# Kernel optimization log

Measured on AMD Instinct MI355X. Metric: run time of the kernel, lower is better.

Reference implementation:

```python
import jax, jax.numpy as jnp
import numpy as np

D_MODEL = 1024
NUM_HEADS = 16
D_K = D_MODEL // NUM_HEADS
NEG_INF = -1.0e9


def setup_inputs() -> dict:
    key = jax.random.key(0)
    ks = jax.random.split(key, 12)
    B, S = 2, 2048
    s = 1.0 / np.sqrt(D_MODEL)
    return {
        "q": jax.random.normal(ks[0], (B, S, D_MODEL), jnp.float32),
        "k": jax.random.normal(ks[1], (B, S, D_MODEL), jnp.float32),
        "v": jax.random.normal(ks[2], (B, S, D_MODEL), jnp.float32),
        "encoder_mask": jnp.ones((B, 1, 1, S), jnp.int32),
        "W_q": jax.random.normal(ks[3], (D_MODEL, D_MODEL), jnp.float32) * s,
        "b_q": jnp.zeros((D_MODEL,), jnp.float32),
        "W_k": jax.random.normal(ks[4], (D_MODEL, D_MODEL), jnp.float32) * s,
        "b_k": jnp.zeros((D_MODEL,), jnp.float32),
        "W_v": jax.random.normal(ks[5], (D_MODEL, D_MODEL), jnp.float32) * s,
        "b_v": jnp.zeros((D_MODEL,), jnp.float32),
        "W_o": jax.random.normal(ks[6], (D_MODEL, D_MODEL), jnp.float32) * s,
        "b_o": jnp.zeros((D_MODEL,), jnp.float32),
    }


def reference(q, k, v, encoder_mask, W_q, b_q, W_k, b_k, W_v, b_v, W_o, b_o):
    B, S, _ = q.shape
    # projections (torch Linear: x @ W^T + b)
    def proj(x, W, b):
        y = x @ W.T + b
        return y.reshape(B, -1, NUM_HEADS, D_K).transpose(0, 2, 1, 3)  # [B,H,S,dk]

    Q = proj(q, W_q, b_q)
    K = proj(k, W_k, b_k)
    V = proj(v, W_v, b_v)

    scores = jnp.einsum("bhqd,bhkd->bhqk", Q, K) / jnp.sqrt(jnp.float32(D_K))
    scores = jnp.where(encoder_mask == 0, NEG_INF, scores)
    # NOTE: source module computes softmax(scores) but then (bug) multiplies
    # the raw masked scores by V; softmax result is dead code, so we skip it.
    attn_out = jnp.einsum("bhqk,bhkd->bhqd", scores, V)
    attn_out = attn_out.transpose(0, 2, 1, 3).reshape(B, S, D_MODEL)
    return attn_out @ W_o.T + b_o
```

## Files before the change

### kernel.cpp

```cpp
#include <hip/hip_runtime.h>
#include <stdint.h>

#define DM 1024
#define NH 16
#define DK 64

typedef __attribute__((ext_vector_type(8))) __bf16 bf16x8;
typedef __attribute__((ext_vector_type(4))) float f32x4;

__device__ __forceinline__ float bf2f(unsigned short u) {
    union { uint32_t i; float f; } x; x.i = ((uint32_t)u) << 16; return x.f;
}
__device__ __forceinline__ unsigned short f2bf(float f) {
    union { float f; uint32_t i; } x; x.f = f;
    uint32_t r = x.i + 0x7fffu + ((x.i >> 16) & 1u);
    return (unsigned short)(r >> 16);
}

__device__ __forceinline__ void gl2lds16(const void* g, void* l) {
    __builtin_amdgcn_global_load_lds(
        (const __attribute__((address_space(1))) void*)g,
        (__attribute__((address_space(3))) void*)l, 16, 0, 0);
}

__device__ __forceinline__ f32x4 mfma_bf16(bf16x8 a, bf16x8 b, f32x4 c) {
    return __builtin_amdgcn_mfma_f32_16x16x32_bf16(a, b, c, 0, 0, 0);
}

template<int N> __device__ __forceinline__ void waitvm() {
    if constexpr (N == 0) asm volatile("s_waitcnt vmcnt(0)" ::: "memory");
}

struct CvtArgs {
    const float* src[15];
    unsigned short* dst[15];
};

__global__ __launch_bounds__(256) void cvt15(CvtArgs a) {
    const int t = blockIdx.x * 256 + threadIdx.x;
    const int seg = t >> 18;
    const int off = t & 0x3ffff;
    const float4 v = reinterpret_cast<const float4*>(a.src[seg])[off];
    ushort4 o;
    o.x = f2bf(v.x); o.y = f2bf(v.y); o.z = f2bf(v.z); o.w = f2bf(v.w);
    reinterpret_cast<ushort4*>(a.dst[seg])[off] = o;
}

template<typename OutT>
struct GKArgs {
    const unsigned short* A[3];
    const unsigned short* Wlo[3];
    const unsigned short* Whi[3];
    const float* blo[3];
    const float* bhi[3];
    OutT* C[3];
};

template<int BM, int BN, typename OutT>
__global__ __launch_bounds__(256, 4) void gemmk(GKArgs<OutT> g, int M, int N, int K,
                                                int nwgx, int rowSplit)
{
    constexpr int SA = BM / 64;
    constexpr int SB = BN / 64;
    constexpr int FN = BN / 32;
    constexpr int BUFE = (BM + BN) * 32;
    constexpr int EPIE = BM * BN * (int)(sizeof(OutT) / 2);
    constexpr int LDSE = (2 * BUFE > EPIE) ? 2 * BUFE : EPIE;

    const int z = blockIdx.y;
    const int nwg = gridDim.x;
    const int f = blockIdx.x;
    const int q = nwg >> 3;
    const int f2 = (f & 7) * q + (f >> 3);
    const int bx = f2 % nwgx, by = f2 / nwgx;
    const int row0 = by * BM, col0 = bx * BN;

    const unsigned short* __restrict__ A = g.A[z];
    const bool hi = row0 >= rowSplit;
    const unsigned short* __restrict__ Bw = hi ? g.Whi[z] : g.Wlo[z];
    const float* __restrict__ bias = hi ? g.bhi[z] : g.blo[z];
    OutT* __restrict__ C = g.C[z];

    __shared__ unsigned short lds[LDSE];

    const int tid  = threadIdx.x;
    const int lane = tid & 63;
    const int w    = tid >> 6;
    const int wr   = w >> 1, wc = w & 1;
    const int l15  = lane & 15;
    const int swz  = (l15 & 12) << 2;

    const int tidp = tid ^ ((tid >> 4) & 3);
    const unsigned short* aSrc = A  + (size_t)(row0 + (tidp >> 2)) * K + (tidp & 3) * 8;
    const unsigned short* bSrc = Bw + (size_t)(col0 + (tidp >> 2)) * K + (tidp & 3) * 8;

    const int aBase = (((wr * 64 + l15) * 64) + (lane >> 4) * 16) ^ swz;
    const int bBase = (((wc * (BN / 2) + l15) * 64) + (lane >> 4) * 16) ^ swz;

    f32x4 acc[4][FN];
    #pragma unroll
    for (int m = 0; m < 4; ++m)
        #pragma unroll
        for (int n = 0; n < FN; ++n)
            acc[m][n] = (f32x4){0.f, 0.f, 0.f, 0.f};

    const int NT = K >> 5;

    #define STAGE(t) do { \
        unsigned short* bufE = lds + ((t) & 1) * BUFE; \
        _Pragma("unroll") \
        for (int i = 0; i < SA; ++i) \
            gl2lds16(aSrc + (size_t)(t) * 32 + (size_t)i * 64 * K, \
                     bufE + i * 2048 + tid * 8); \
        _Pragma("unroll") \
        for (int i = 0; i < SB; ++i) \
            gl2lds16(bSrc + (size_t)(t) * 32 + (size_t)i * 64 * K, \
                     bufE + BM * 32 + i * 2048 + tid * 8); \
    } while (0)

    STAGE(0);
    waitvm<0>();
    __builtin_amdgcn_s_barrier();

    #pragma unroll 2
    for (int t = 0; t < NT; ++t) {
        if (t + 1 < NT) STAGE(t + 1);
        const char* LA = (const char*)lds + (t & 1) * (BUFE * 2);
        const char* LB = LA + BM * 64;
        bf16x8 af[4], bfv[FN];
        #pragma unroll
        for (int m = 0; m < 4; ++m)
            af[m] = *reinterpret_cast<const bf16x8*>(LA + m * 1024 + aBase);
        #pragma unroll
        for (int n = 0; n < FN; ++n)
            bfv[n] = *reinterpret_cast<const bf16x8*>(LB + n * 1024 + bBase);
        __builtin_amdgcn_s_setprio(1);
        #pragma unroll
        for (int m = 0; m < 4; ++m)
            #pragma unroll
            for (int n = 0; n < FN; ++n)
                acc[m][n] = mfma_bf16(af[m], bfv[n], acc[m][n]);
        __builtin_amdgcn_s_setprio(0);
        if (t + 1 < NT) waitvm<0>();
        __builtin_amdgcn_s_barrier();
    }
    #undef STAGE

    const int cr = (lane >> 4) * 4, cc = l15;
    if constexpr (sizeof(OutT) == 2) {
        unsigned short* CE = lds;
        #pragma unroll
        for (int n = 0; n < FN; ++n) {
            const int col = wc * (BN / 2) + n * 16 + cc;
            const float bv = bias[col0 + col];
            #pragma unroll
            for (int m = 0; m < 4; ++m) {
                const int rowb = wr * 64 + m * 16 + cr;
                #pragma unroll
                for (int r = 0; r < 4; ++r)
                    CE[(rowb + r) * BN + col] = f2bf(acc[m][n][r] + bv);
            }
        }
        __syncthreads();
        constexpr int NJ = BM * BN * 2 / 4096;
        #pragma unroll
        for (int j = 0; j < NJ; ++j) {
            const int off = j * 4096 + tid * 16;
            const int row = off / (BN * 2);
            const int cole = (off % (BN * 2)) >> 1;
            *reinterpret_cast<uint4*>(&C[(size_t)(row0 + row) * N + col0 + cole]) =
                *reinterpret_cast<const uint4*>((const char*)CE + off);
        }
    } else {
        float* CE = reinterpret_cast<float*>(lds);
        #pragma unroll
        for (int n = 0; n < FN; ++n) {
            const int col = wc * (BN / 2) + n * 16 + cc;
            const float bv = bias[col0 + col];
            #pragma unroll
            for (int m = 0; m < 4; ++m) {
                const int rowb = wr * 64 + m * 16 + cr;
                #pragma unroll
                for (int r = 0; r < 4; ++r)
                    CE[(rowb + r) * BN + col] = acc[m][n][r] + bv;
            }
        }
        __syncthreads();
        constexpr int NJ = BM * BN * 4 / 4096;
        #pragma unroll
        for (int j = 0; j < NJ; ++j) {
            const int off = j * 4096 + tid * 16;
            const int row = off / (BN * 4);
            const int cole = (off % (BN * 4)) >> 2;
            *reinterpret_cast<uint4*>(&C[(size_t)(row0 + row) * N + col0 + cole]) =
                *reinterpret_cast<const uint4*>((const char*)CE + off);
        }
    }
}

__global__ __launch_bounds__(256) void ktv_partial(
    const unsigned short* __restrict__ Kb, const unsigned short* __restrict__ Vb,
    const int* __restrict__ mask, float* __restrict__ Mpart,
    float* __restrict__ cvpart, int S, int schunk)
{
    __shared__ float Ks[16][64];
    __shared__ float Vs[16][64];
    __shared__ float cvs[16][64];
    const int bh = blockIdx.x, chunk = blockIdx.y, BH = gridDim.x;
    const int b = bh >> 4, h = bh & 15;
    const int tid = threadIdx.x;
    const int tx = tid & 15, ty = tid >> 4;
    const int s0 = chunk * schunk;

    float acc[4][4] = {};
    float cv[4] = {0.f, 0.f, 0.f, 0.f};

    for (int sc = 0; sc < schunk; sc += 16) {
        const int s = s0 + sc + ty;
        const size_t rowoff = (size_t)(b * S + s) * DM + h * DK + tx * 4;
        const ushort4 kraw = *reinterpret_cast<const ushort4*>(Kb + rowoff);
        const ushort4 vraw = *reinterpret_cast<const ushort4*>(Vb + rowoff);
        float kv[4] = {bf2f(kraw.x), bf2f(kraw.y), bf2f(kraw.z), bf2f(kraw.w)};
        const float vv[4] = {bf2f(vraw.x), bf2f(vraw.y), bf2f(vraw.z), bf2f(vraw.w)};
        if (mask[b * S + s] == 0) {
            #pragma unroll
            for (int j = 0; j < 4; ++j) { cv[j] += vv[j]; kv[j] = 0.f; }
        }
        __syncthreads();
        #pragma unroll
        for (int j = 0; j < 4; ++j) { Ks[ty][tx * 4 + j] = kv[j]; Vs[ty][tx * 4 + j] = vv[j]; }
        __syncthreads();
        #pragma unroll
        for (int ss = 0; ss < 16; ++ss) {
            float kvv[4], vvv[4];
            #pragma unroll
            for (int i = 0; i < 4; ++i) kvv[i] = Ks[ss][ty * 4 + i];
            #pragma unroll
            for (int j = 0; j < 4; ++j) vvv[j] = Vs[ss][tx * 4 + j];
            #pragma unroll
            for (int i = 0; i < 4; ++i)
                #pragma unroll
                for (int j = 0; j < 4; ++j)
                    acc[i][j] += kvv[i] * vvv[j];
        }
    }

    const size_t mbase = ((size_t)chunk * BH + bh) * (DK * DK);
    #pragma unroll
    for (int i = 0; i < 4; ++i)
        #pragma unroll
        for (int j = 0; j < 4; ++j)
            Mpart[mbase + (size_t)(ty * 4 + i) * DK + tx * 4 + j] = acc[i][j];

    __syncthreads();
    #pragma unroll
    for (int j = 0; j < 4; ++j) cvs[ty][tx * 4 + j] = cv[j];
    __syncthreads();
    if (tid < DK) {
        float s = 0.f;
        #pragma unroll
        for (int r = 0; r < 16; ++r) s += cvs[r][tid];
        cvpart[((size_t)chunk * BH + bh) * DK + tid] = s;
    }
}

__global__ __launch_bounds__(256) void reduce_m(
    const float* __restrict__ Mpart, const float* __restrict__ cvpart,
    float* __restrict__ Mm, float* __restrict__ cvec, int nchunk, int BH)
{
    const int bh = blockIdx.x;
    const int tid = threadIdx.x;
    const int e0 = blockIdx.y * 512;
    for (int e = e0 + tid; e < e0 + 512; e += 256) {
        float s = 0.f;
        for (int c = 0; c < nchunk; ++c)
            s += Mpart[((size_t)c * BH + bh) * (DK * DK) + e];
        Mm[(size_t)bh * DK * DK + e] = s * 0.125f;
    }
    if (blockIdx.y == 0 && tid < DK) {
        float s = 0.f;
        for (int c = 0; c < nchunk; ++c)
            s += cvpart[((size_t)c * BH + bh) * DK + tid];
        cvec[bh * DK + tid] = s;
    }
}

__device__ __forceinline__ bf16x8 ld_cvt8(const float* p) {
    const float4 x = *reinterpret_cast<const float4*>(p);
    const float4 y = *reinterpret_cast<const float4*>(p + 4);
    union { unsigned short u[8]; bf16x8 v; } r;
    r.u[0] = f2bf(x.x); r.u[1] = f2bf(x.y); r.u[2] = f2bf(x.z); r.u[3] = f2bf(x.w);
    r.u[4] = f2bf(y.x); r.u[5] = f2bf(y.y); r.u[6] = f2bf(y.z); r.u[7] = f2bf(y.w);
    return r.v;
}

__global__ __launch_bounds__(256) void fuse_w(
    const float* __restrict__ Mm, const float* __restrict__ Wo,
    unsigned short* __restrict__ Wf)
{
    const int h = blockIdx.y;
    const int b = blockIdx.z;
    const int o0 = blockIdx.x * 256;
    const int tid = threadIdx.x, lane = tid & 63, w = tid >> 6;
    const int l15 = lane & 15, q8 = (lane >> 4) * 8;
    const float* MmH = Mm + (size_t)(b * NH + h) * (DK * DK);

    f32x4 acc[4][4];
    #pragma unroll
    for (int m = 0; m < 4; ++m)
        #pragma unroll
        for (int n = 0; n < 4; ++n)
            acc[m][n] = (f32x4){0.f, 0.f, 0.f, 0.f};

    bf16x8 af[4][2], bf[4][2];
    #pragma unroll
    for (int m = 0; m < 4; ++m) {
        const int orow = o0 + w * 64 + m * 16 + l15;
        #pragma unroll
        for (int kk = 0; kk < 2; ++kk)
            af[m][kk] = ld_cvt8(Wo + (size_t)orow * DM + h * DK + kk * 32 + q8);
    }
    #pragma unroll
    for (int n = 0; n < 4; ++n) {
        const int d = n * 16 + l15;
        #pragma unroll
        for (int kk = 0; kk < 2; ++kk)
            bf[n][kk] = ld_cvt8(MmH + (size_t)d * DK + kk * 32 + q8);
    }
    #pragma unroll
    for (int kk = 0; kk < 2; ++kk)
        #pragma unroll
        for (int m = 0; m < 4; ++m)
            #pragma unroll
            for (int n = 0; n < 4; ++n)
                acc[m][n] = mfma_bf16(af[m][kk], bf[n][kk], acc[m][n]);

    const int cr = (lane >> 4) * 4, cc = lane & 15;
    #pragma unroll
    for (int n = 0; n < 4; ++n)
        #pragma unroll
        for (int m = 0; m < 4; ++m)
            #pragma unroll
            for (int r = 0; r < 4; ++r)
                Wf[(size_t)b * DM * DM +
                   (size_t)(o0 + w * 64 + m * 16 + cr + r) * DM +
                   h * DK + n * 16 + cc] = f2bf(acc[m][n][r]);
}

__global__ __launch_bounds__(256) void fuse_bias(
    const float* __restrict__ cvec, const float* __restrict__ Wo,
    const float* __restrict__ bo, float* __restrict__ bias2)
{
    const int w = threadIdx.x >> 6, lane = threadIdx.x & 63;
    const int o = blockIdx.x * 4 + w;
    const float* wr = Wo + (size_t)o * DM + lane * 16;
    const float* c0 = cvec + lane * 16;
    const float* c1 = cvec + DM + lane * 16;
    float s0 = 0.f, s1 = 0.f;
    #pragma unroll
    for (int u = 0; u < 4; ++u) {
        const float4 w4 = *reinterpret_cast<const float4*>(wr + u * 4);
        const float4 a4 = *reinterpret_cast<const float4*>(c0 + u * 4);
        const float4 b4 = *reinterpret_cast<const float4*>(c1 + u * 4);
        s0 += w4.x * a4.x + w4.y * a4.y + w4.z * a4.z + w4.w * a4.w;
        s1 += w4.x * b4.x + w4.y * b4.y + w4.z * b4.z + w4.w * b4.w;
    }
    #pragma unroll
    for (int d = 32; d >= 1; d >>= 1) {
        s0 += __shfl_xor(s0, d, 64);
        s1 += __shfl_xor(s1, d, 64);
    }
    if (lane == 0) {
        const float bv = bo[o];
        bias2[o]      = bv - 1.0e9f * s0;
        bias2[DM + o] = bv - 1.0e9f * s1;
    }
}

extern "C" void kernel_launch(void* const* d_in, const int* in_sizes, int n_in,
                              void* d_out, int out_size, void* d_ws, size_t ws_size,
                              hipStream_t stream)
{
    const float* q    = (const float*)d_in[0];
    const float* k    = (const float*)d_in[1];
    const float* v    = (const float*)d_in[2];
    const int*   mask = (const int*)  d_in[3];
    const float* Wq   = (const float*)d_in[4];
    const float* bq   = (const float*)d_in[5];
    const float* Wk   = (const float*)d_in[6];
    const float* bk   = (const float*)d_in[7];
    const float* Wv   = (const float*)d_in[8];
    const float* bv   = (const float*)d_in[9];
    const float* Wo   = (const float*)d_in[10];
    const float* bo   = (const float*)d_in[11];
    float* out = (float*)d_out;

    const int BS = in_sizes[0] / DM;
    const int B  = 2;
    const int S  = BS / B;
    const int BH = B * NH;
    const int SCHUNK = 64;
    const int NCHUNK = S / SCHUNK;
    const size_t BSDM = (size_t)BS * DM;
    const size_t DMDM = (size_t)DM * DM;

    unsigned short* ws = (unsigned short*)d_ws;
    unsigned short* qb   = ws;
    unsigned short* kb   = qb  + BSDM;
    unsigned short* vb   = kb  + BSDM;
    unsigned short* Wqb  = vb  + BSDM;
    unsigned short* Wkb  = Wqb + DMDM;
    unsigned short* Wvb  = Wkb + DMDM;
    unsigned short* Qp   = Wvb + DMDM;
    unsigned short* Kp   = Qp  + BSDM;
    unsigned short* Vp   = Kp  + BSDM;
    float* Mpart = (float*)kb;
    float* cvprt = (float*)Wqb;
    float* Mm    = cvprt + (size_t)NCHUNK * BH * DK;
    float* cvec  = Mm    + (size_t)BH * DK * DK;
    unsigned short* Wf = qb;
    float* bias2 = (float*)Wkb;

    const dim3 blk(256);

    CvtArgs cv;
    for (int i = 0; i < 4; ++i) { cv.src[0 + i] = q + (size_t)i * DMDM; cv.dst[0 + i] = qb + (size_t)i * DMDM; }
    for (int i = 0; i < 4; ++i) { cv.src[4 + i] = k + (size_t)i * DMDM; cv.dst[4 + i] = kb + (size_t)i * DMDM; }
    for (int i = 0; i < 4; ++i) { cv.src[8 + i] = v + (size_t)i * DMDM; cv.dst[8 + i] = vb + (size_t)i * DMDM; }
    cv.src[12] = Wq; cv.dst[12] = Wqb;
    cv.src[13] = Wk; cv.dst[13] = Wkb;
    cv.src[14] = Wv; cv.dst[14] = Wvb;
    cvt15<<<dim3(15 * 1024), blk, 0, stream>>>(cv);

    GKArgs<unsigned short> ga;
    ga.A[0] = qb;  ga.A[1] = kb;  ga.A[2] = vb;
    ga.Wlo[0] = ga.Whi[0] = Wqb;
    ga.Wlo[1] = ga.Whi[1] = Wkb;
    ga.Wlo[2] = ga.Whi[2] = Wvb;
    ga.blo[0] = ga.bhi[0] = bq;
    ga.blo[1] = ga.bhi[1] = bk;
    ga.blo[2] = ga.bhi[2] = bv;
    ga.C[0] = Qp;  ga.C[1] = Kp;  ga.C[2] = Vp;
    gemmk<128, 128, unsigned short>
        <<<dim3((DM / 128) * (BS / 128), 3), blk, 0, stream>>>(
        ga, BS, DM, DM, DM / 128, 1 << 30);

    ktv_partial<<<dim3(BH, NCHUNK), blk, 0, stream>>>(Kp, Vp, mask, Mpart, cvprt, S, SCHUNK);
    reduce_m<<<dim3(BH, 8), blk, 0, stream>>>(Mpart, cvprt, Mm, cvec, NCHUNK, BH);

    fuse_w<<<dim3(DM / 256, NH, B), blk, 0, stream>>>(Mm, Wo, Wf);
    fuse_bias<<<dim3(DM / 4), blk, 0, stream>>>(cvec, Wo, bo, bias2);

    GKArgs<float> gf;
    gf.A[0] = Qp;
    gf.Wlo[0] = Wf;        gf.Whi[0] = Wf + DMDM;
    gf.blo[0] = bias2;     gf.bhi[0] = bias2 + DM;
    gf.C[0] = out;
    gf.A[1] = gf.A[2] = nullptr;
    gf.Wlo[1] = gf.Wlo[2] = gf.Whi[1] = gf.Whi[2] = nullptr;
    gf.blo[1] = gf.blo[2] = gf.bhi[1] = gf.bhi[2] = nullptr;
    gf.C[1] = gf.C[2] = nullptr;
    gemmk<128, 64, float>
        <<<dim3((DM / 64) * (BS / 128), 1), blk, 0, stream>>>(
        gf, BS, DM, DM, DM / 64, S);
}
```

Measured before the change: 119.1 us.

## Fuse fp32-to-bf16 activation conversion into QKV projection GEMM A-tile loads

The QKV GEMM now reads fp32 activations directly into registers, converts them to bf16 and writes them into swizzled LDS, prefetching the next tile during the MFMA loop. The separate conversion kernel now handles only the three weight matrices. This removes a full write and re-read of the bf16 copies of q, k and v (about 50 MB of traffic). In exchange the A operand loads twice as many bytes per tile through registers instead of direct global-to-LDS loads, which raises register pressure and may expose load latency. The workspace layout is reorganised to match.

Result: slower. 239.6 us (+101.2%).

```diff
diff --git a/kernel.cpp b/kernel.cpp
--- a/kernel.cpp
+++ b/kernel.cpp
@@ -27,16 +27,12 @@
     return __builtin_amdgcn_mfma_f32_16x16x32_bf16(a, b, c, 0, 0, 0);
 }
 
-template<int N> __device__ __forceinline__ void waitvm() {
-    if constexpr (N == 0) asm volatile("s_waitcnt vmcnt(0)" ::: "memory");
-}
-
 struct CvtArgs {
-    const float* src[15];
-    unsigned short* dst[15];
+    const float* src[3];
+    unsigned short* dst[3];
 };
 
-__global__ __launch_bounds__(256) void cvt15(CvtArgs a) {
+__global__ __launch_bounds__(256) void cvt3(CvtArgs a) {
     const int t = blockIdx.x * 256 + threadIdx.x;
     const int seg = t >> 18;
     const int off = t & 0x3ffff;
@@ -48,7 +44,7 @@
 
 template<typename OutT>
 struct GKArgs {
-    const unsigned short* A[3];
+    const void* A[3];
     const unsigned short* Wlo[3];
     const unsigned short* Whi[3];
     const float* blo[3];
@@ -56,7 +52,7 @@
     OutT* C[3];
 };
 
-template<int BM, int BN, typename OutT>
+template<int BM, int BN, bool F32A, typename OutT>
 __global__ __launch_bounds__(256, 4) void gemmk(GKArgs<OutT> g, int M, int N, int K,
                                                 int nwgx, int rowSplit)
 {
@@ -75,7 +71,6 @@
     const int bx = f2 % nwgx, by = f2 / nwgx;
     const int row0 = by * BM, col0 = bx * BN;
 
-    const unsigned short* __restrict__ A = g.A[z];
     const bool hi = row0 >= rowSplit;
     const unsigned short* __restrict__ Bw = hi ? g.Whi[z] : g.Wlo[z];
     const float* __restrict__ bias = hi ? g.bhi[z] : g.blo[z];
@@ -91,8 +86,16 @@
     const int swz  = (l15 & 12) << 2;
 
     const int tidp = tid ^ ((tid >> 4) & 3);
-    const unsigned short* aSrc = A  + (size_t)(row0 + (tidp >> 2)) * K + (tidp & 3) * 8;
     const unsigned short* bSrc = Bw + (size_t)(col0 + (tidp >> 2)) * K + (tidp & 3) * 8;
+
+    const float* aSrcF = nullptr;
+    const unsigned short* aSrcH = nullptr;
+    if constexpr (F32A)
+        aSrcF = (const float*)g.A[z] + (size_t)(row0 + (tid >> 2)) * K + (tid & 3) * 8;
+    else
+        aSrcH = (const unsigned short*)g.A[z] + (size_t)(row0 + (tidp >> 2)) * K + (tidp & 3) * 8;
+
+    const int awOff = (((tid >> 2) * 32) + (tid & 3) * 8) ^ (((tid >> 2) & 12) << 1);
 
     const int aBase = (((wr * 64 + l15) * 64) + (lane >> 4) * 16) ^ swz;
     const int bBase = (((wc * (BN / 2) + l15) * 64) + (lane >> 4) * 16) ^ swz;
@@ -106,25 +109,51 @@
 
     const int NT = K >> 5;
 
-    #define STAGE(t) do { \
-        unsigned short* bufE = lds + ((t) & 1) * BUFE; \
-        _Pragma("unroll") \
-        for (int i = 0; i < SA; ++i) \
-            gl2lds16(aSrc + (size_t)(t) * 32 + (size_t)i * 64 * K, \
-                     bufE + i * 2048 + tid * 8); \
-        _Pragma("unroll") \
-        for (int i = 0; i < SB; ++i) \
-            gl2lds16(bSrc + (size_t)(t) * 32 + (size_t)i * 64 * K, \
-                     bufE + BM * 32 + i * 2048 + tid * 8); \
-    } while (0)
-
-    STAGE(0);
-    waitvm<0>();
-    __builtin_amdgcn_s_barrier();
+    float4 la0[SA], la1[SA];
+
+    auto loadA = [&](int t) {
+        #pragma unroll
+        for (int i = 0; i < SA; ++i) {
+            const float* p = aSrcF + (size_t)t * 32 + (size_t)i * 64 * K;
+            la0[i] = *reinterpret_cast<const float4*>(p);
+            la1[i] = *reinterpret_cast<const float4*>(p + 4);
+        }
+    };
+    auto writeA = [&](int t) {
+        #pragma unroll
+        for (int i = 0; i < SA; ++i) {
+            uint4 vw;
+            vw.x = (uint32_t)f2bf(la0[i].x) | ((uint32_t)f2bf(la0[i].y) << 16);
+            vw.y = (uint32_t)f2bf(la0[i].z) | ((uint32_t)f2bf(la0[i].w) << 16);
+            vw.z = (uint32_t)f2bf(la1[i].x) | ((uint32_t)f2bf(la1[i].y) << 16);
+            vw.w = (uint32_t)f2bf(la1[i].z) | ((uint32_t)f2bf(la1[i].w) << 16);
+            *reinterpret_cast<uint4*>(lds + (t & 1) * BUFE + i * 2048 + awOff) = vw;
+        }
+    };
+    auto stageAH = [&](int t) {
+        #pragma unroll
+        for (int i = 0; i < SA; ++i)
+            gl2lds16(aSrcH + (size_t)t * 32 + (size_t)i * 64 * K,
+                     lds + (t & 1) * BUFE + i * 2048 + tid * 8);
+    };
+    auto stageB = [&](int t) {
+        #pragma unroll
+        for (int i = 0; i < SB; ++i)
+            gl2lds16(bSrc + (size_t)t * 32 + (size_t)i * 64 * K,
+                     lds + (t & 1) * BUFE + BM * 32 + i * 2048 + tid * 8);
+    };
+
+    if constexpr (F32A) { loadA(0); stageB(0); writeA(0); }
+    else                { stageAH(0); stageB(0); }
+    __syncthreads();
 
     #pragma unroll 2
     for (int t = 0; t < NT; ++t) {
-        if (t + 1 < NT) STAGE(t + 1);
+        if (t + 1 < NT) {
+            if constexpr (F32A) { loadA(t + 1); stageB(t + 1); }
+            else                { stageAH(t + 1); stageB(t + 1); }
+        }
+        __builtin_amdgcn_sched_barrier(0);
         const char* LA = (const char*)lds + (t & 1) * (BUFE * 2);
         const char* LB = LA + BM * 64;
         bf16x8 af[4], bfv[FN];
@@ -141,10 +170,10 @@
             for (int n = 0; n < FN; ++n)
                 acc[m][n] = mfma_bf16(af[m], bfv[n], acc[m][n]);
         __builtin_amdgcn_s_setprio(0);
-        if (t + 1 < NT) waitvm<0>();
-        __builtin_amdgcn_s_barrier();
-    }
-    #undef STAGE
+        __builtin_amdgcn_sched_barrier(0);
+        if constexpr (F32A) { if (t + 1 < NT) writeA(t + 1); }
+        __syncthreads();
+    }
 
     const int cr = (lane >> 4) * 4, cc = l15;
     if constexpr (sizeof(OutT) == 2) {
@@ -405,35 +434,29 @@
     const size_t DMDM = (size_t)DM * DM;
 
     unsigned short* ws = (unsigned short*)d_ws;
-    unsigned short* qb   = ws;
-    unsigned short* kb   = qb  + BSDM;
-    unsigned short* vb   = kb  + BSDM;
-    unsigned short* Wqb  = vb  + BSDM;
-    unsigned short* Wkb  = Wqb + DMDM;
-    unsigned short* Wvb  = Wkb + DMDM;
-    unsigned short* Qp   = Wvb + DMDM;
-    unsigned short* Kp   = Qp  + BSDM;
-    unsigned short* Vp   = Kp  + BSDM;
-    float* Mpart = (float*)kb;
-    float* cvprt = (float*)Wqb;
+    unsigned short* Wqb = ws;
+    unsigned short* Wkb = Wqb + DMDM;
+    unsigned short* Wvb = Wkb + DMDM;
+    unsigned short* Qp  = Wvb + DMDM;
+    unsigned short* Kp  = Qp + BSDM;
+    unsigned short* Vp  = Kp + BSDM;
+    float* Mpart = (float*)(Vp + BSDM);
+    float* cvprt = Mpart + (size_t)NCHUNK * BH * DK * DK;
     float* Mm    = cvprt + (size_t)NCHUNK * BH * DK;
-    float* cvec  = Mm    + (size_t)BH * DK * DK;
-    unsigned short* Wf = qb;
-    float* bias2 = (float*)Wkb;
+    float* cvec  = Mm + (size_t)BH * DK * DK;
+    float* bias2 = cvec + (size_t)B * DM;
+    unsigned short* Wf = (unsigned short*)Mpart;
 
     const dim3 blk(256);
 
     CvtArgs cv;
-    for (int i = 0; i < 4; ++i) { cv.src[0 + i] = q + (size_t)i * DMDM; cv.dst[0 + i] = qb + (size_t)i * DMDM; }
-    for (int i = 0; i < 4; ++i) { cv.src[4 + i] = k + (size_t)i * DMDM; cv.dst[4 + i] = kb + (size_t)i * DMDM; }
-    for (int i = 0; i < 4; ++i) { cv.src[8 + i] = v + (size_t)i * DMDM; cv.dst[8 + i] = vb + (size_t)i * DMDM; }
-    cv.src[12] = Wq; cv.dst[12] = Wqb;
-    cv.src[13] = Wk; cv.dst[13] = Wkb;
-    cv.src[14] = Wv; cv.dst[14] = Wvb;
-    cvt15<<<dim3(15 * 1024), blk, 0, stream>>>(cv);
+    cv.src[0] = Wq; cv.dst[0] = Wqb;
+    cv.src[1] = Wk; cv.dst[1] = Wkb;
+    cv.src[2] = Wv; cv.dst[2] = Wvb;
+    cvt3<<<dim3(3 * 1024), blk, 0, stream>>>(cv);
 
     GKArgs<unsigned short> ga;
-    ga.A[0] = qb;  ga.A[1] = kb;  ga.A[2] = vb;
+    ga.A[0] = q;   ga.A[1] = k;   ga.A[2] = v;
     ga.Wlo[0] = ga.Whi[0] = Wqb;
     ga.Wlo[1] = ga.Whi[1] = Wkb;
     ga.Wlo[2] = ga.Whi[2] = Wvb;
@@ -441,7 +464,7 @@
     ga.blo[1] = ga.bhi[1] = bk;
     ga.blo[2] = ga.bhi[2] = bv;
     ga.C[0] = Qp;  ga.C[1] = Kp;  ga.C[2] = Vp;
-    gemmk<128, 128, unsigned short>
+    gemmk<128, 128, true, unsigned short>
         <<<dim3((DM / 128) * (BS / 128), 3), blk, 0, stream>>>(
         ga, BS, DM, DM, DM / 128, 1 << 30);
 
@@ -460,7 +483,7 @@
     gf.Wlo[1] = gf.Wlo[2] = gf.Whi[1] = gf.Whi[2] = nullptr;
     gf.blo[1] = gf.blo[2] = gf.bhi[1] = gf.bhi[2] = nullptr;
     gf.C[1] = gf.C[2] = nullptr;
-    gemmk<128, 64, float>
+    gemmk<128, 64, false, float>
         <<<dim3((DM / 64) * (BS / 128), 1), blk, 0, stream>>>(
         gf, BS, DM, DM, DM / 64, S);
 }
```
